# Kernel tuning notes

Hardware: AMD Instinct MI355X
Metric: run time of the kernel (lower is better)

The kernel has to match this reference:

```python
import jax, jax.numpy as jnp
import numpy as np

NUM_HEADS = 12


def setup_inputs() -> dict:
    key = jax.random.key(0)
    ks = jax.random.split(key, 6)
    B, N, C, CNN = 64, 576, 768, 2048
    return {
        "image_patches": jax.random.normal(ks[0], (B, N, C), dtype=jnp.float32),
        "cnn_feature_vector": jax.random.normal(ks[1], (B, CNN), dtype=jnp.float32),
        "Wq": jax.random.normal(ks[2], (C, C), dtype=jnp.float32) * (C ** -0.5),
        "Wkv": jax.random.normal(ks[3], (CNN, 2 * C), dtype=jnp.float32) * (CNN ** -0.5),
        "Wp": jax.random.normal(ks[4], (C, C), dtype=jnp.float32) * (C ** -0.5),
        "bp": jnp.zeros((C,), dtype=jnp.float32),
    }


def reference(image_patches, cnn_feature_vector, Wq, Wkv, Wp, bp):
    B, N, C = image_patches.shape
    H = NUM_HEADS
    D = C // H
    scale = D ** -0.5
    # Q projection: [B, N, C] -> [B, N, H, D]
    q = (image_patches @ Wq).reshape(B, N, H, D)
    # KV projection from single CNN feature (KV seq len == 1): [B, 2C]
    kv = cnn_feature_vector @ Wkv
    k = kv[:, :C].reshape(B, H, D)  # [B, H, D]
    v = kv[:, C:].reshape(B, H, D)  # [B, H, D]
    # attn logits: q . k over head_dim -> [B, N, H, 1]; softmax over kv_len=1
    logits = jnp.einsum("bnhd,bhd->bnh", q, k)[..., None] * scale
    attn = jax.nn.softmax(logits, axis=-1)  # degenerate: all ones
    # attn @ v with kv_len 1 -> broadcast v over N
    x = (attn * v[:, None, :, :]).reshape(B, N, C)
    # output projection (dropout is identity in eval)
    return x @ Wp + bp
```

## Files before the change

kernel.cpp:

```cpp
#include <hip/hip_runtime.h>


#define B_DIM   64
#define N_DIM   576
#define C_DIM   768
#define CNN_DIM 2048
#define C4_DIM  192

__global__ __launch_bounds__(256) void gemm1_kernel(
    const float* __restrict__ cnn, const float* __restrict__ Wkv,
    float* __restrict__ v)
{
    int gid = blockIdx.x * 256 + threadIdx.x;
    int c4 = gid % C4_DIM;
    int bg = (gid / C4_DIM) % 8;
    int s  = gid / (C4_DIM * 8);
    int b0 = bg * 8;
    int k0 = s * 64;

    const float4* w4 = (const float4*)(Wkv + C_DIM);

    float4 acc[8];
#pragma unroll
    for (int i = 0; i < 8; ++i) acc[i] = make_float4(0.f, 0.f, 0.f, 0.f);

#pragma unroll 4
    for (int kk = 0; kk < 64; ++kk) {
        int k = k0 + kk;
        float4 w = w4[k * 384 + c4];
#pragma unroll
        for (int i = 0; i < 8; ++i) {
            float a = cnn[(b0 + i) * CNN_DIM + k];
            acc[i].x = fmaf(a, w.x, acc[i].x);
            acc[i].y = fmaf(a, w.y, acc[i].y);
            acc[i].z = fmaf(a, w.z, acc[i].z);
            acc[i].w = fmaf(a, w.w, acc[i].w);
        }
    }

#pragma unroll
    for (int i = 0; i < 8; ++i) {
        float* dst = v + (b0 + i) * C_DIM + c4 * 4;
        unsafeAtomicAdd(dst + 0, acc[i].x);
        unsafeAtomicAdd(dst + 1, acc[i].y);
        unsafeAtomicAdd(dst + 2, acc[i].z);
        unsafeAtomicAdd(dst + 3, acc[i].w);
    }
}

__global__ __launch_bounds__(256) void gemm2_kernel(
    const float* __restrict__ v, const float* __restrict__ Wp,
    float* __restrict__ y)
{
    int gid = blockIdx.x * 256 + threadIdx.x;
    int c4 = gid % C4_DIM;
    int bg = (gid / C4_DIM) % 8;
    int s  = gid / (C4_DIM * 8);
    int b0 = bg * 8;
    int k0 = s * 32;

    const float4* w4 = (const float4*)Wp;

    float4 acc[8];
#pragma unroll
    for (int i = 0; i < 8; ++i) acc[i] = make_float4(0.f, 0.f, 0.f, 0.f);

#pragma unroll 4
    for (int kk = 0; kk < 32; ++kk) {
        int k = k0 + kk;
        float4 w = w4[k * C4_DIM + c4];
#pragma unroll
        for (int i = 0; i < 8; ++i) {
            float a = v[(b0 + i) * C_DIM + k];
            acc[i].x = fmaf(a, w.x, acc[i].x);
            acc[i].y = fmaf(a, w.y, acc[i].y);
            acc[i].z = fmaf(a, w.z, acc[i].z);
            acc[i].w = fmaf(a, w.w, acc[i].w);
        }
    }

#pragma unroll
    for (int i = 0; i < 8; ++i) {
        float* dst = y + (b0 + i) * C_DIM + c4 * 4;
        unsafeAtomicAdd(dst + 0, acc[i].x);
        unsafeAtomicAdd(dst + 1, acc[i].y);
        unsafeAtomicAdd(dst + 2, acc[i].z);
        unsafeAtomicAdd(dst + 3, acc[i].w);
    }
}

__global__ __launch_bounds__(256) void bcast_kernel(
    const float* __restrict__ y, const float* __restrict__ bp,
    float4* __restrict__ out)
{
    int idx = blockIdx.x * 256 + threadIdx.x;
    int c4 = idx % C4_DIM;
    int b  = idx / (N_DIM * C4_DIM);
    float4 r  = *(const float4*)(y + b * C_DIM + c4 * 4);
    float4 bb = *(const float4*)(bp + c4 * 4);
    r.x += bb.x; r.y += bb.y; r.z += bb.z; r.w += bb.w;
    out[idx] = r;
}

extern "C" void kernel_launch(void* const* d_in, const int* in_sizes, int n_in,
                              void* d_out, int out_size, void* d_ws, size_t ws_size,
                              hipStream_t stream)
{
    const float* cnn = (const float*)d_in[1];
    const float* Wkv = (const float*)d_in[3];
    const float* Wp  = (const float*)d_in[4];
    const float* bp  = (const float*)d_in[5];

    float* v = (float*)d_ws;
    float* y = v + B_DIM * C_DIM;

    hipMemsetAsync(d_ws, 0, (size_t)2 * B_DIM * C_DIM * sizeof(float), stream);

    gemm1_kernel<<<192, 256, 0, stream>>>(cnn, Wkv, v);
    gemm2_kernel<<<144, 256, 0, stream>>>(v, Wp, y);

    int n_out4 = B_DIM * N_DIM * C4_DIM;
    bcast_kernel<<<n_out4 / 256, 256, 0, stream>>>(y, bp, (float4*)d_out);
}
```

Before: 275.1 us.

## Replace atomic split-K with in-block LDS reduction, fold bias, nontemporal broadcast stores

Both small GEMMs now place the whole K-split for a tile inside one block and sum the partials through a shared-memory tree reduction, instead of spreading the split across blocks and combining with global atomics. This lets the workspace memset and the atomics go away. The bias add moves into the second projection, and the broadcast kernel writes the large output with nontemporal stores. The trade-off is extra __syncthreads steps and 32KB of LDS per block, and proj_y now uses 24-wide K slices.

```diff
diff --git a/kernel.cpp b/kernel.cpp
--- a/kernel.cpp
+++ b/kernel.cpp
@@ -7,99 +7,125 @@
 #define CNN_DIM 2048
 #define C4_DIM  192
 
-__global__ __launch_bounds__(256) void gemm1_kernel(
+typedef float f4 __attribute__((ext_vector_type(4)));
+
+__global__ __launch_bounds__(256) void proj_v_kernel(
     const float* __restrict__ cnn, const float* __restrict__ Wkv,
     float* __restrict__ v)
 {
-    int gid = blockIdx.x * 256 + threadIdx.x;
-    int c4 = gid % C4_DIM;
-    int bg = (gid / C4_DIM) % 8;
-    int s  = gid / (C4_DIM * 8);
-    int b0 = bg * 8;
-    int k0 = s * 64;
+    __shared__ f4 red[32 * 64];
 
-    const float4* w4 = (const float4*)(Wkv + C_DIM);
+    int tid = threadIdx.x;
+    int c4l = tid & 7;
+    int s   = tid >> 3;
+    int bg  = blockIdx.x & 7;
+    int cg  = blockIdx.x >> 3;
+    int b0  = bg * 8;
+    int c4  = cg * 8 + c4l;
+    int k0  = s * 64;
 
-    float4 acc[8];
+    const f4* w4 = (const f4*)(Wkv + C_DIM);
+
+    f4 acc[8];
 #pragma unroll
-    for (int i = 0; i < 8; ++i) acc[i] = make_float4(0.f, 0.f, 0.f, 0.f);
+    for (int i = 0; i < 8; ++i) acc[i] = (f4)0.f;
 
 #pragma unroll 4
     for (int kk = 0; kk < 64; ++kk) {
         int k = k0 + kk;
-        float4 w = w4[k * 384 + c4];
+        f4 w = w4[k * 384 + c4];
 #pragma unroll
         for (int i = 0; i < 8; ++i) {
             float a = cnn[(b0 + i) * CNN_DIM + k];
-            acc[i].x = fmaf(a, w.x, acc[i].x);
-            acc[i].y = fmaf(a, w.y, acc[i].y);
-            acc[i].z = fmaf(a, w.z, acc[i].z);
-            acc[i].w = fmaf(a, w.w, acc[i].w);
+            acc[i] += a * w;
         }
     }
 
 #pragma unroll
-    for (int i = 0; i < 8; ++i) {
-        float* dst = v + (b0 + i) * C_DIM + c4 * 4;
-        unsafeAtomicAdd(dst + 0, acc[i].x);
-        unsafeAtomicAdd(dst + 1, acc[i].y);
-        unsafeAtomicAdd(dst + 2, acc[i].z);
-        unsafeAtomicAdd(dst + 3, acc[i].w);
+    for (int i = 0; i < 8; ++i) red[s * 64 + i * 8 + c4l] = acc[i];
+    __syncthreads();
+
+#pragma unroll
+    for (int step = 16; step >= 1; step >>= 1) {
+        if (s < step) {
+#pragma unroll
+            for (int i = 0; i < 8; ++i)
+                red[s * 64 + i * 8 + c4l] += red[(s + step) * 64 + i * 8 + c4l];
+        }
+        __syncthreads();
+    }
+
+    if (tid < 64) {
+        int i  = tid >> 3;
+        int cl = tid & 7;
+        *(f4*)(v + (b0 + i) * C_DIM + (cg * 8 + cl) * 4) = red[i * 8 + cl];
     }
 }
 
-__global__ __launch_bounds__(256) void gemm2_kernel(
+__global__ __launch_bounds__(256) void proj_y_kernel(
     const float* __restrict__ v, const float* __restrict__ Wp,
-    float* __restrict__ y)
+    const float* __restrict__ bp, float* __restrict__ y)
 {
-    int gid = blockIdx.x * 256 + threadIdx.x;
-    int c4 = gid % C4_DIM;
-    int bg = (gid / C4_DIM) % 8;
-    int s  = gid / (C4_DIM * 8);
-    int b0 = bg * 8;
-    int k0 = s * 32;
+    __shared__ f4 red[32 * 64];
 
-    const float4* w4 = (const float4*)Wp;
+    int tid = threadIdx.x;
+    int c4l = tid & 7;
+    int s   = tid >> 3;
+    int bg  = blockIdx.x & 7;
+    int cg  = blockIdx.x >> 3;
+    int b0  = bg * 8;
+    int c4  = cg * 8 + c4l;
+    int k0  = s * 24;
 
-    float4 acc[8];
+    const f4* w4 = (const f4*)Wp;
+
+    f4 acc[8];
 #pragma unroll
-    for (int i = 0; i < 8; ++i) acc[i] = make_float4(0.f, 0.f, 0.f, 0.f);
+    for (int i = 0; i < 8; ++i) acc[i] = (f4)0.f;
 
 #pragma unroll 4
-    for (int kk = 0; kk < 32; ++kk) {
+    for (int kk = 0; kk < 24; ++kk) {
         int k = k0 + kk;
-        float4 w = w4[k * C4_DIM + c4];
+        f4 w = w4[k * C4_DIM + c4];
 #pragma unroll
         for (int i = 0; i < 8; ++i) {
             float a = v[(b0 + i) * C_DIM + k];
-            acc[i].x = fmaf(a, w.x, acc[i].x);
-            acc[i].y = fmaf(a, w.y, acc[i].y);
-            acc[i].z = fmaf(a, w.z, acc[i].z);
-            acc[i].w = fmaf(a, w.w, acc[i].w);
+            acc[i] += a * w;
         }
     }
 
 #pragma unroll
-    for (int i = 0; i < 8; ++i) {
-        float* dst = y + (b0 + i) * C_DIM + c4 * 4;
-        unsafeAtomicAdd(dst + 0, acc[i].x);
-        unsafeAtomicAdd(dst + 1, acc[i].y);
-        unsafeAtomicAdd(dst + 2, acc[i].z);
-        unsafeAtomicAdd(dst + 3, acc[i].w);
+    for (int i = 0; i < 8; ++i) red[s * 64 + i * 8 + c4l] = acc[i];
+    __syncthreads();
+
+#pragma unroll
+    for (int step = 16; step >= 1; step >>= 1) {
+        if (s < step) {
+#pragma unroll
+            for (int i = 0; i < 8; ++i)
+                red[s * 64 + i * 8 + c4l] += red[(s + step) * 64 + i * 8 + c4l];
+        }
+        __syncthreads();
+    }
+
+    if (tid < 64) {
+        int i  = tid >> 3;
+        int cl = tid & 7;
+        f4 r  = red[i * 8 + cl];
+        f4 bb = *(const f4*)(bp + (cg * 8 + cl) * 4);
+        r += bb;
+        *(f4*)(y + (b0 + i) * C_DIM + (cg * 8 + cl) * 4) = r;
     }
 }
 
 __global__ __launch_bounds__(256) void bcast_kernel(
-    const float* __restrict__ y, const float* __restrict__ bp,
-    float4* __restrict__ out)
+    const f4* __restrict__ y4, f4* __restrict__ out)
 {
     int idx = blockIdx.x * 256 + threadIdx.x;
-    int c4 = idx % C4_DIM;
-    int b  = idx / (N_DIM * C4_DIM);
-    float4 r  = *(const float4*)(y + b * C_DIM + c4 * 4);
-    float4 bb = *(const float4*)(bp + c4 * 4);
-    r.x += bb.x; r.y += bb.y; r.z += bb.z; r.w += bb.w;
-    out[idx] = r;
+    int c4  = idx % C4_DIM;
+    int b   = idx / (N_DIM * C4_DIM);
+    f4 r = y4[b * C4_DIM + c4];
+    __builtin_nontemporal_store(r, &out[idx]);
 }
 
 extern "C" void kernel_launch(void* const* d_in, const int* in_sizes, int n_in,
@@ -114,11 +140,9 @@
     float* v = (float*)d_ws;
     float* y = v + B_DIM * C_DIM;
 
-    hipMemsetAsync(d_ws, 0, (size_t)2 * B_DIM * C_DIM * sizeof(float), stream);
-
-    gemm1_kernel<<<192, 256, 0, stream>>>(cnn, Wkv, v);
-    gemm2_kernel<<<144, 256, 0, stream>>>(v, Wp, y);
+    proj_v_kernel<<<192, 256, 0, stream>>>(cnn, Wkv, v);
+    proj_y_kernel<<<192, 256, 0, stream>>>(v, Wp, bp, y);
 
     int n_out4 = B_DIM * N_DIM * C4_DIM;
-    bcast_kernel<<<n_out4 / 256, 256, 0, stream>>>(y, bp, (float4*)d_out);
+    bcast_kernel<<<n_out4 / 256, 256, 0, stream>>>((const f4*)y, (f4*)d_out);
 }
```

Result: faster. 232.5 us (-15.5%).
